# Optimization experiments

Hardware: AMD Instinct MI355X
Metric: run time of the kernel (lower is better)

## Reference

```python
import jax, jax.numpy as jnp
import numpy as np


def _haar_filters():
    h = 1.0 / np.sqrt(2.0)
    rec_lo = np.array([h, h], dtype=np.float32)
    rec_hi = np.array([h, -h], dtype=np.float32)
    # torch: w_xy[i, j] = rec_y[i] * rec_x[j] (unsqueeze(1) gives rows)
    w_ll = rec_lo[:, None] * rec_lo[None, :]
    w_hl = rec_lo[:, None] * rec_hi[None, :]
    w_lh = rec_hi[:, None] * rec_lo[None, :]
    w_hh = rec_hi[:, None] * rec_hi[None, :]
    return jnp.asarray(np.stack([w_ll, w_lh, w_hl, w_hh], axis=0))  # [4,2,2]


def setup_inputs() -> dict:
    key = jax.random.key(0)
    B, Ct, H, W = 4, 256, 256, 256  # Ct = 4 * 64 wavelet groups
    x = jax.random.normal(key, (B, Ct, H, W), dtype=jnp.float32)
    filters = _haar_filters()
    return {"x": x, "filters": filters}


def reference(x, filters):
    # x: [B, 4C, H, W]; filters: [4, 2, 2]
    B, Ct, H, W = x.shape
    C = Ct // 4
    # rearrange 'b (n c) h w -> b (c n) h w'
    xp = x.reshape(B, 4, C, H, W).transpose(0, 2, 1, 3, 4)  # [B, C, 4, H, W]
    # conv_transpose2d with weight expand(4C, 4, 2, 2), groups=C:
    # every input channel in a group uses the same 4 kernels, so each group's
    # 4 output channels are filters[j] scattered from the SUM over the group.
    s = xp.sum(axis=2)  # [B, C, H, W]
    # stride-2, 2x2 kernel transpose conv == non-overlapping pixel-shuffle scatter:
    # y[b, g*4+j, 2h+a, 2w+c] = s[b, g, h, w] * filters[j, a, c]
    y = jnp.einsum('bghw,jac->bgjhawc', s, filters)  # [B,C,4,H,2,W,2]
    return y.reshape(B, Ct, 2 * H, 2 * W)
```

## Files before the change

### kernel.cpp

```cpp
#include <hip/hip_runtime.h>


#define B   4
#define C   64
#define H   256
#define W   256
#define W4  (W / 4)

__global__ __launch_bounds__(256) void idwt2d_haar_kernel(
    const float* __restrict__ x,
    const float* __restrict__ filt,
    float* __restrict__ y)
{
    const int tid = blockIdx.x * 256 + threadIdx.x;
    const int w4 = tid & (W4 - 1);
    const int h  = (tid >> 6) & (H - 1);
    const int g  = (tid >> 14) & (C - 1);
    const int b  = tid >> 20;

    const int w = w4 << 2;

    const int nstride = C * H * W;
    const int in_base = (((b * (4 * C)) + g) * H + h) * W + w;
    const float4 x0 = *(const float4*)(x + in_base);
    const float4 x1 = *(const float4*)(x + in_base + nstride);
    const float4 x2 = *(const float4*)(x + in_base + 2 * nstride);
    const float4 x3 = *(const float4*)(x + in_base + 3 * nstride);

    float4 s;
    s.x = (x0.x + x1.x) + (x2.x + x3.x);
    s.y = (x0.y + x1.y) + (x2.y + x3.y);
    s.z = (x0.z + x1.z) + (x2.z + x3.z);
    s.w = (x0.w + x1.w) + (x2.w + x3.w);

    const int out_ch0 = b * (4 * C) + g * 4;
    const int row0 = 2 * h;
    const int col0 = 2 * w;

#pragma unroll
    for (int j = 0; j < 4; ++j) {
        const float fj00 = filt[j * 4 + 0];
        const float fj01 = filt[j * 4 + 1];
        const float fj10 = filt[j * 4 + 2];
        const float fj11 = filt[j * 4 + 3];
        const int ch_base = ((out_ch0 + j) * (2 * H)) * (2 * W);
#pragma unroll
        for (int a = 0; a < 2; ++a) {
            const float f0 = (a == 0) ? fj00 : fj10;
            const float f1 = (a == 0) ? fj01 : fj11;
            float4 o0, o1;
            o0.x = s.x * f0; o0.y = s.x * f1;
            o0.z = s.y * f0; o0.w = s.y * f1;
            o1.x = s.z * f0; o1.y = s.z * f1;
            o1.z = s.w * f0; o1.w = s.w * f1;
            const int off = ch_base + (row0 + a) * (2 * W) + col0;
            *(float4*)(y + off)     = o0;
            *(float4*)(y + off + 4) = o1;
        }
    }
}

extern "C" void kernel_launch(void* const* d_in, const int* in_sizes, int n_in,
                              void* d_out, int out_size, void* d_ws, size_t ws_size,
                              hipStream_t stream) {
    const float* x    = (const float*)d_in[0];
    const float* filt = (const float*)d_in[1];
    float* y = (float*)d_out;

    const int total_threads = B * C * H * W4;
    const int block = 256;
    const int grid = total_threads / block;
    idwt2d_haar_kernel<<<grid, block, 0, stream>>>(x, filt, y);
}
```

Baseline: 1.233 ms.

## Stage group sums in LDS for contiguous wave stores, use nontemporal loads/stores

Each block now sums 16 input rows of one wavelet group into shared memory, then remaps threads so each wavefront writes contiguous 1KB spans of an output row for one filter channel. Before, each lane wrote 32B pieces scattered across four channels. Loads and stores also become nontemporal, to avoid polluting the cache with streaming data. The cost is an LDS round trip plus a barrier per block.

```diff
diff --git a/kernel.cpp b/kernel.cpp
--- a/kernel.cpp
+++ b/kernel.cpp
@@ -5,57 +5,74 @@
 #define C   64
 #define H   256
 #define W   256
-#define W4  (W / 4)
+#define R   16
+#define OW  (2 * W)
+#define OH  (2 * H)
+
+typedef float f2 __attribute__((ext_vector_type(2)));
+typedef float f4 __attribute__((ext_vector_type(4)));
 
 __global__ __launch_bounds__(256) void idwt2d_haar_kernel(
     const float* __restrict__ x,
     const float* __restrict__ filt,
     float* __restrict__ y)
 {
-    const int tid = blockIdx.x * 256 + threadIdx.x;
-    const int w4 = tid & (W4 - 1);
-    const int h  = (tid >> 6) & (H - 1);
-    const int g  = (tid >> 14) & (C - 1);
-    const int b  = tid >> 20;
+    __shared__ float s_lds[R][W];
 
-    const int w = w4 << 2;
+    const int t   = threadIdx.x;
+    const int bid = blockIdx.x;
+    const int hb  = bid & (H / R - 1);
+    const int g   = (bid >> 4) & (C - 1);
+    const int b   = bid >> 10;
+    const int h0  = hb * R;
 
+    const int w4 = t & 63;
+    const int rq = t >> 6;
     const int nstride = C * H * W;
-    const int in_base = (((b * (4 * C)) + g) * H + h) * W + w;
-    const float4 x0 = *(const float4*)(x + in_base);
-    const float4 x1 = *(const float4*)(x + in_base + nstride);
-    const float4 x2 = *(const float4*)(x + in_base + 2 * nstride);
-    const float4 x3 = *(const float4*)(x + in_base + 3 * nstride);
-
-    float4 s;
-    s.x = (x0.x + x1.x) + (x2.x + x3.x);
-    s.y = (x0.y + x1.y) + (x2.y + x3.y);
-    s.z = (x0.z + x1.z) + (x2.z + x3.z);
-    s.w = (x0.w + x1.w) + (x2.w + x3.w);
-
-    const int out_ch0 = b * (4 * C) + g * 4;
-    const int row0 = 2 * h;
-    const int col0 = 2 * w;
 
 #pragma unroll
-    for (int j = 0; j < 4; ++j) {
-        const float fj00 = filt[j * 4 + 0];
-        const float fj01 = filt[j * 4 + 1];
-        const float fj10 = filt[j * 4 + 2];
-        const float fj11 = filt[j * 4 + 3];
-        const int ch_base = ((out_ch0 + j) * (2 * H)) * (2 * W);
+    for (int rr = 0; rr < 4; ++rr) {
+        const int r = rq + 4 * rr;
+        const int base = (((b * (4 * C)) + g) * H + (h0 + r)) * W + 4 * w4;
+        const f4 x0 = __builtin_nontemporal_load((const f4*)(x + base));
+        const f4 x1 = __builtin_nontemporal_load((const f4*)(x + base + nstride));
+        const f4 x2 = __builtin_nontemporal_load((const f4*)(x + base + 2 * nstride));
+        const f4 x3 = __builtin_nontemporal_load((const f4*)(x + base + 3 * nstride));
+        f4 s;
+        s.x = (x0.x + x1.x) + (x2.x + x3.x);
+        s.y = (x0.y + x1.y) + (x2.y + x3.y);
+        s.z = (x0.z + x1.z) + (x2.z + x3.z);
+        s.w = (x0.w + x1.w) + (x2.w + x3.w);
+        *(f4*)&s_lds[r][4 * w4] = s;
+    }
+    __syncthreads();
+
+    const int j = t >> 6;
+    const int L = t & 63;
+
+    const float fj00 = filt[j * 4 + 0];
+    const float fj01 = filt[j * 4 + 1];
+    const float fj10 = filt[j * 4 + 2];
+    const float fj11 = filt[j * 4 + 3];
+
+    float* p = y + (((b * (4 * C)) + (g * 4 + j)) * OH + 2 * h0) * OW;
+
+#pragma unroll
+    for (int r = 0; r < R; ++r) {
+        const f2 sa = *(const f2*)&s_lds[r][2 * L];
+        const f2 sb = *(const f2*)&s_lds[r][128 + 2 * L];
 #pragma unroll
         for (int a = 0; a < 2; ++a) {
-            const float f0 = (a == 0) ? fj00 : fj10;
-            const float f1 = (a == 0) ? fj01 : fj11;
-            float4 o0, o1;
-            o0.x = s.x * f0; o0.y = s.x * f1;
-            o0.z = s.y * f0; o0.w = s.y * f1;
-            o1.x = s.z * f0; o1.y = s.z * f1;
-            o1.z = s.w * f0; o1.w = s.w * f1;
-            const int off = ch_base + (row0 + a) * (2 * W) + col0;
-            *(float4*)(y + off)     = o0;
-            *(float4*)(y + off + 4) = o1;
+            const float f0 = a ? fj10 : fj00;
+            const float f1 = a ? fj11 : fj01;
+            f4 oA, oB;
+            oA.x = sa.x * f0; oA.y = sa.x * f1;
+            oA.z = sa.y * f0; oA.w = sa.y * f1;
+            oB.x = sb.x * f0; oB.y = sb.x * f1;
+            oB.z = sb.y * f0; oB.w = sb.y * f1;
+            __builtin_nontemporal_store(oA, (f4*)(p + 4 * L));
+            __builtin_nontemporal_store(oB, (f4*)(p + 256 + 4 * L));
+            p += OW;
         }
     }
 }
@@ -67,8 +84,6 @@
     const float* filt = (const float*)d_in[1];
     float* y = (float*)d_out;
 
-    const int total_threads = B * C * H * W4;
-    const int block = 256;
-    const int grid = total_threads / block;
-    idwt2d_haar_kernel<<<grid, block, 0, stream>>>(x, filt, y);
+    const int grid = B * C * (H / R);
+    idwt2d_haar_kernel<<<grid, 256, 0, stream>>>(x, filt, y);
 }
```

New measurement: 1.220 ms. No clear change (-1.0%).
